# Performance work log

Measured on AMD Instinct MI355X. Metric: run time of the kernel, lower is better.

The kernel has to match this reference:

```python
import jax, jax.numpy as jnp
import numpy as np

D_MODEL = 1024
NHEAD = 16
HEAD_DIM = D_MODEL // NHEAD
D_FF = 4096
B, S = 2, 2048
LN_EPS = 1e-5


def _linear_params(key, d_out, d_in):
    kw, kb = jax.random.split(key)
    lim = 1.0 / np.sqrt(d_in)
    W = jax.random.uniform(kw, (d_out, d_in), jnp.float32, -lim, lim)
    b = jax.random.uniform(kb, (d_out,), jnp.float32, -lim, lim)
    return W, b


def setup_inputs() -> dict:
    key = jax.random.key(0)
    ks = jax.random.split(key, 8)
    src = jax.random.normal(ks[0], (B, S, D_MODEL), jnp.float32)
    mask = jax.random.randint(ks[1], (B, S), 0, 2).astype(bool)
    Wq, bq = _linear_params(ks[2], D_MODEL, D_MODEL)
    Wk, bk = _linear_params(ks[3], D_MODEL, D_MODEL)
    Wv, bv = _linear_params(ks[4], D_MODEL, D_MODEL)
    Wo, bo = _linear_params(ks[5], D_MODEL, D_MODEL)
    W1, b1 = _linear_params(ks[6], D_FF, D_MODEL)
    W2, b2 = _linear_params(ks[7], D_MODEL, D_FF)
    ln1_g = jnp.ones((D_MODEL,), jnp.float32)
    ln1_b = jnp.zeros((D_MODEL,), jnp.float32)
    ln2_g = jnp.ones((D_MODEL,), jnp.float32)
    ln2_b = jnp.zeros((D_MODEL,), jnp.float32)
    return dict(src=src, mask=mask, Wq=Wq, bq=bq, Wk=Wk, bk=bk, Wv=Wv, bv=bv,
                Wo=Wo, bo=bo, W1=W1, b1=b1, W2=W2, b2=b2,
                ln1_g=ln1_g, ln1_b=ln1_b, ln2_g=ln2_g, ln2_b=ln2_b)


def _layernorm(x, g, b):
    mu = jnp.mean(x, axis=-1, keepdims=True)
    var = jnp.mean(jnp.square(x - mu), axis=-1, keepdims=True)
    return (x - mu) * jax.lax.rsqrt(var + LN_EPS) * g + b


def reference(src, mask, Wq, bq, Wk, bk, Wv, bv, Wo, bo, W1, b1, W2, b2,
              ln1_g, ln1_b, ln2_g, ln2_b):
    batch, seq, _ = src.shape
    src_norm = _layernorm(src, ln1_g, ln1_b)
    # projections (torch Linear: x @ W.T + b), split heads -> [B,H,S,Dh]
    def proj(W, b):
        y = jnp.einsum('bsi,oi->bso', src_norm, W) + b
        return y.reshape(batch, seq, NHEAD, HEAD_DIM).transpose(0, 2, 1, 3)
    q, k, v = proj(Wq, bq), proj(Wk, bk), proj(Wv, bv)
    scores = jnp.einsum('bhqd,bhkd->bhqk', q, k) / np.sqrt(HEAD_DIM)
    scores = jnp.where(mask[:, None, None, :], -10000.0, scores)
    attn_probs = jax.nn.softmax(scores, axis=-1)
    attn_out = jnp.einsum('bhqk,bhkd->bhqd', attn_probs, v)
    attn_out = attn_out.transpose(0, 2, 1, 3).reshape(batch, seq, D_MODEL)
    attn_out = jnp.einsum('bsi,oi->bso', attn_out, Wo) + bo
    src = src + attn_out
    src_norm2 = _layernorm(src, ln2_g, ln2_b)
    h = jax.nn.relu(jnp.einsum('bsi,oi->bso', src_norm2, W1) + b1)
    ff = jnp.einsum('bsi,oi->bso', h, W2) + b2
    src = src + ff
    return (src, attn_probs)
```

## Files before the change

kernel.cpp:

```cpp
#include <hip/hip_runtime.h>
#include <math.h>

typedef __bf16 bf16;
typedef __bf16 bf16x4 __attribute__((ext_vector_type(4)));
typedef __bf16 bf16x8 __attribute__((ext_vector_type(8)));
typedef float f32x4 __attribute__((ext_vector_type(4)));

__device__ __forceinline__ f32x4 mfma16(bf16x8 a, bf16x8 b, f32x4 c) {
  return __builtin_amdgcn_mfma_f32_16x16x32_bf16(a, b, c, 0, 0, 0);
}

__device__ __forceinline__ void gload_lds16(const void* g, void* l) {
  __builtin_amdgcn_global_load_lds((__attribute__((address_space(1))) void*)(g),
                                   (__attribute__((address_space(3))) void*)(l),
                                   16, 0, 0);
}

__global__ __launch_bounds__(256)
void cvt_all(const float* __restrict__ Wq, const float* __restrict__ Wk,
             const float* __restrict__ Wv, const float* __restrict__ Wo,
             const float* __restrict__ W1, const float* __restrict__ W2,
             const float* __restrict__ bq, const float* __restrict__ bk,
             const float* __restrict__ bv, bf16* __restrict__ wqkv,
             bf16* __restrict__ wob, bf16* __restrict__ w1b,
             bf16* __restrict__ w2b, float* __restrict__ bqkv) {
  const int i = blockIdx.x * 256 + threadIdx.x;
  if (i < 3145728) {
    float4 v;
    bf16* dst;
    size_t di;
    if (i < 262144) { v = ((const float4*)Wq)[i]; dst = wqkv; di = i; }
    else if (i < 524288) { v = ((const float4*)Wk)[i - 262144]; dst = wqkv; di = i; }
    else if (i < 786432) { v = ((const float4*)Wv)[i - 524288]; dst = wqkv; di = i; }
    else if (i < 1048576) { v = ((const float4*)Wo)[i - 786432]; dst = wob; di = i - 786432; }
    else if (i < 2097152) { v = ((const float4*)W1)[i - 1048576]; dst = w1b; di = i - 1048576; }
    else { v = ((const float4*)W2)[i - 2097152]; dst = w2b; di = i - 2097152; }
    bf16x4 o;
    o[0] = (bf16)v.x; o[1] = (bf16)v.y; o[2] = (bf16)v.z; o[3] = (bf16)v.w;
    reinterpret_cast<bf16x4*>(dst)[di] = o;
  } else {
    const int j = i - 3145728;
    const float* s = (j < 256) ? bq : ((j < 512) ? bk : bv);
    reinterpret_cast<float4*>(bqkv)[j] = reinterpret_cast<const float4*>(s)[j & 255];
  }
}

__global__ __launch_bounds__(256)
void ln_bf16(const float* __restrict__ x, const float* __restrict__ g,
             const float* __restrict__ bta, bf16* __restrict__ y) {
  const int row = blockIdx.x, t = threadIdx.x;
  const float4 v = reinterpret_cast<const float4*>(x)[(size_t)row * 256 + t];
  float s1 = v.x + v.y + v.z + v.w;
  float s2 = v.x * v.x + v.y * v.y + v.z * v.z + v.w * v.w;
#pragma unroll
  for (int m = 1; m < 64; m <<= 1) {
    s1 += __shfl_xor(s1, m);
    s2 += __shfl_xor(s2, m);
  }
  __shared__ float red[8];
  if ((t & 63) == 0) { red[(t >> 6) * 2] = s1; red[(t >> 6) * 2 + 1] = s2; }
  __syncthreads();
  s1 = red[0] + red[2] + red[4] + red[6];
  s2 = red[1] + red[3] + red[5] + red[7];
  const float mu = s1 * (1.f / 1024.f);
  const float rs = rsqrtf(s2 * (1.f / 1024.f) - mu * mu + 1e-5f);
  const float4 gv = reinterpret_cast<const float4*>(g)[t];
  const float4 bv = reinterpret_cast<const float4*>(bta)[t];
  bf16x4 o;
  o[0] = (bf16)((v.x - mu) * rs * gv.x + bv.x);
  o[1] = (bf16)((v.y - mu) * rs * gv.y + bv.y);
  o[2] = (bf16)((v.z - mu) * rs * gv.z + bv.z);
  o[3] = (bf16)((v.w - mu) * rs * gv.w + bv.w);
  reinterpret_cast<bf16x4*>(y)[(size_t)row * 256 + t] = o;
}

__global__ __launch_bounds__(256)
void tr_v(const bf16* __restrict__ QKV, bf16* __restrict__ VT) {
  __shared__ bf16 T[64 * 80];
  const int t = threadIdx.x;
  const int sb = blockIdx.x * 64, h = blockIdx.y, b = blockIdx.z;
  const int srow = t >> 2, c16 = t & 3;
  const bf16* src = QKV + (size_t)(b * 2048 + sb + srow) * 3072 + 2048 + h * 64 + c16 * 16;
  bf16x8 a0 = *reinterpret_cast<const bf16x8*>(src);
  bf16x8 a1 = *reinterpret_cast<const bf16x8*>(src + 8);
  *reinterpret_cast<bf16x8*>(&T[srow * 80 + c16 * 16]) = a0;
  *reinterpret_cast<bf16x8*>(&T[srow * 80 + c16 * 16 + 8]) = a1;
  __syncthreads();
  const int drow = t >> 2, sq = t & 3;
  bf16x8 o0, o1;
#pragma unroll
  for (int j = 0; j < 8; ++j) o0[j] = T[(sq * 16 + j) * 80 + drow];
#pragma unroll
  for (int j = 0; j < 8; ++j) o1[j] = T[(sq * 16 + 8 + j) * 80 + drow];
  bf16* dst = VT + ((size_t)(b * 16 + h) * 64 + drow) * 2048 + sb + sq * 16;
  *reinterpret_cast<bf16x8*>(dst) = o0;
  *reinterpret_cast<bf16x8*>(dst + 8) = o1;
}

template <int TM, bool OUT_BF16, bool RELU, bool RES, bool QSC>
__global__ __launch_bounds__(256)
void gemm_bt(const bf16* __restrict__ A, const bf16* __restrict__ Bw,
             const float* __restrict__ bias, const float* __restrict__ res,
             void* __restrict__ Cout, int M, int N, int K) {
  constexpr int MR = TM / 32;
  constexpr int ACH = TM / 64;
  __shared__ bf16 As[3][TM * 32];
  __shared__ bf16 Bs[3][128 * 32];
  const int t = threadIdx.x, wave = t >> 6, lane = t & 63;
  const int l15 = lane & 15, lhi = lane >> 4;
  const int nwg = gridDim.x * gridDim.y;
  const int orig = blockIdx.y * gridDim.x + blockIdx.x;
  const int wgid = (orig & 7) * (nwg >> 3) + (orig >> 3);
  const int bx = wgid % gridDim.x, by = wgid / gridDim.x;
  const int m0 = by * TM, n0 = bx * 128;
  const int wm = (wave >> 1) * (TM / 2), wn = (wave & 1) * 64;
  const f32x4 z4 = {0.f, 0.f, 0.f, 0.f};
  f32x4 acc[MR][4];
#pragma unroll
  for (int m = 0; m < MR; ++m)
#pragma unroll
    for (int n = 0; n < 4; ++n) acc[m][n] = z4;

  int soff[2], srow[2], scol[2];
#pragma unroll
  for (int i = 0; i < 2; ++i) {
    soff[i] = (i * 4 + wave) * 1024 + lane * 16;
    srow[i] = soff[i] >> 6;
    scol[i] = (soff[i] & 63) >> 1;
  }

#define GEMM_STAGE(k0, bb)                                                    \
  do {                                                                        \
    _Pragma("unroll")                                                         \
    for (int i = 0; i < ACH; ++i)                                             \
      gload_lds16(A + (size_t)(m0 + srow[i]) * K + (k0) + scol[i],            \
                  (char*)As[bb] + soff[i]);                                   \
    _Pragma("unroll")                                                         \
    for (int i = 0; i < 2; ++i)                                               \
      gload_lds16(Bw + (size_t)(n0 + srow[i]) * K + (k0) + scol[i],           \
                  (char*)Bs[bb] + soff[i]);                                   \
  } while (0)

  const int nt = K >> 5;
  GEMM_STAGE(0, 0);
  GEMM_STAGE(32, 1);
  if constexpr (TM == 128)
    asm volatile("s_waitcnt vmcnt(4)" ::: "memory");
  else
    asm volatile("s_waitcnt vmcnt(3)" ::: "memory");
  __builtin_amdgcn_s_barrier();

  for (int kt = 0; kt < nt; ++kt) {
    if (kt + 2 < nt) GEMM_STAGE((kt + 2) * 32, (kt + 2) % 3);
    const bf16* Ac = As[kt % 3];
    const bf16* Bc = Bs[kt % 3];
    bf16x8 af[MR], bfr[4];
#pragma unroll
    for (int m = 0; m < MR; ++m)
      af[m] = *reinterpret_cast<const bf16x8*>(&Ac[(wm + m * 16 + l15) * 32 + lhi * 8]);
#pragma unroll
    for (int n = 0; n < 4; ++n)
      bfr[n] = *reinterpret_cast<const bf16x8*>(&Bc[(wn + n * 16 + l15) * 32 + lhi * 8]);
    __builtin_amdgcn_s_setprio(1);
#pragma unroll
    for (int m = 0; m < MR; ++m)
#pragma unroll
      for (int n = 0; n < 4; ++n) acc[m][n] = mfma16(af[m], bfr[n], acc[m][n]);
    __builtin_amdgcn_s_setprio(0);
    if (kt + 1 < nt) {
      if (kt + 2 < nt) {
        if constexpr (TM == 128)
          asm volatile("s_waitcnt vmcnt(4)" ::: "memory");
        else
          asm volatile("s_waitcnt vmcnt(3)" ::: "memory");
      } else {
        asm volatile("s_waitcnt vmcnt(0)" ::: "memory");
      }
      __builtin_amdgcn_s_barrier();
    }
  }
#undef GEMM_STAGE

  const float sc = (QSC && n0 < 1024) ? 0.18033688011112042f : 1.0f;
#pragma unroll
  for (int m = 0; m < MR; ++m) {
    const int row_base = m0 + wm + m * 16 + lhi * 4;
#pragma unroll
    for (int n = 0; n < 4; ++n) {
      const int col = n0 + wn + n * 16 + l15;
      const float bv = bias[col];
#pragma unroll
      for (int r = 0; r < 4; ++r) {
        const int row = row_base + r;
        float v = (acc[m][n][r] + bv) * sc;
        if (RELU) v = v > 0.f ? v : 0.f;
        if (RES) v += res[(size_t)row * N + col];
        if (OUT_BF16)
          ((bf16*)Cout)[(size_t)row * N + col] = (bf16)v;
        else
          ((float*)Cout)[(size_t)row * N + col] = v;
      }
    }
  }
}

__global__ __launch_bounds__(512)
void attn_fused2(const bf16* __restrict__ Qp, const bf16* __restrict__ Kp,
                 const bf16* __restrict__ VTp, const int* __restrict__ mask,
                 float* __restrict__ probs, bf16* __restrict__ Ob) {
  constexpr int S = 2048, LD = 3072, KB = 128, NT = S / KB;
  __shared__ bf16 Kt[KB * 64];
  __shared__ bf16 Vt[64 * KB];
  __shared__ bf16 P[128 * KB];
  __shared__ float msk2[2][KB];
  const int t = threadIdx.x, wave = t >> 6, lane = t & 63;
  const int l15 = lane & 15, lhi = lane >> 4;
  const int flat = blockIdx.x + 16 * (blockIdx.y + 16 * blockIdx.z);
  const int wg = (flat & 7) * 64 + (flat >> 3);
  const int q0 = (wg & 15) * 128, h = (wg >> 4) & 15, b = wg >> 8;
  const int* mrow = mask + b * S;
  const f32x4 z4 = {0.f, 0.f, 0.f, 0.f};

  const bf16* kgp[2];
  const bf16* vgp[2];
  int soff[2];
#pragma unroll
  for (int i = 0; i < 2; ++i) {
    const int off = (i * 8 + wave) * 1024 + lane * 16;
    soff[i] = off;
    const int krow = off >> 7, kbin = off & 127;
    kgp[i] = Kp + (size_t)(b * S + krow) * LD + h * 64 + ((kbin ^ ((krow & 7) << 4)) >> 1);
    const int d = off >> 8, vbin = off & 255;
    vgp[i] = VTp + (size_t)((b * 16 + h) * 64 + d) * S + ((vbin ^ ((d & 7) << 4)) >> 1);
  }

  bf16x8 qf[2];
#pragma unroll
  for (int ks = 0; ks < 2; ++ks)
    qf[ks] = *reinterpret_cast<const bf16x8*>(
        Qp + (size_t)(b * S + q0 + wave * 16 + l15) * LD + h * 64 + ks * 32 + lhi * 8);

  bf16x8 kreg[2];
  float mnext;
#pragma unroll
  for (int i = 0; i < 2; ++i) kreg[i] = *reinterpret_cast<const bf16x8*>(kgp[i]);
  mnext = (t < KB) ? (mrow[t] ? 0.f : 1.f) : 0.f;
#pragma unroll
  for (int i = 0; i < 2; ++i)
    *reinterpret_cast<bf16x8*>((char*)Kt + soff[i]) = kreg[i];
  if (t < KB) msk2[0][t] = mnext;
  __syncthreads();

  float lpart = 0.f;
  for (int kt = 0; kt < NT; ++kt) {
    const int kv0 = kt * KB;
    if (kt + 1 < NT) {
#pragma unroll
      for (int i = 0; i < 2; ++i)
        kreg[i] = *reinterpret_cast<const bf16x8*>(kgp[i] + (size_t)(kv0 + KB) * LD);
      mnext = (t < KB) ? (mrow[kv0 + KB + t] ? 0.f : 1.f) : 0.f;
    }
    const char* kb = (kt & 1) ? (const char*)Vt : (const char*)Kt;
    const float* mc = msk2[kt & 1];
    f32x4 sa[8];
#pragma unroll
    for (int n = 0; n < 8; ++n) sa[n] = z4;
    __builtin_amdgcn_s_setprio(1);
#pragma unroll
    for (int ks = 0; ks < 2; ++ks)
#pragma unroll
      for (int n = 0; n < 8; ++n) {
        const int krow = n * 16 + l15;
        bf16x8 kf = *reinterpret_cast<const bf16x8*>(
            kb + krow * 128 + ((ks * 64 + lhi * 16) ^ ((krow & 7) << 4)));
        sa[n] = mfma16(kf, qf[ks], sa[n]);
      }
    __builtin_amdgcn_s_setprio(0);
#pragma unroll
    for (int n = 0; n < 8; ++n)
#pragma unroll
      for (int r = 0; r < 4; ++r)
        lpart += __builtin_exp2f(sa[n][r]) * mc[n * 16 + lhi * 4 + r];
    if (kt + 1 < NT) {
      char* kbn = ((kt + 1) & 1) ? (char*)Vt : (char*)Kt;
#pragma unroll
      for (int i = 0; i < 2; ++i)
        *reinterpret_cast<bf16x8*>(kbn + soff[i]) = kreg[i];
      if (t < KB) msk2[(kt + 1) & 1][t] = mnext;
    }
    __syncthreads();
  }
  lpart += __shfl_xor(lpart, 16);
  lpart += __shfl_xor(lpart, 32);
  const float il = 1.f / lpart;

  f32x4 oa[4];
#pragma unroll
  for (int n = 0; n < 4; ++n) oa[n] = z4;
  float* pbase = probs + ((size_t)(b * 16 + h) * S + q0 + wave * 16 + l15) * S;
  const int prw = wave * 16 + l15;

  bf16x8 vreg[2];
#pragma unroll
  for (int i = 0; i < 2; ++i) {
    kreg[i] = *reinterpret_cast<const bf16x8*>(kgp[i]);
    vreg[i] = *reinterpret_cast<const bf16x8*>(vgp[i]);
  }
  mnext = (t < KB) ? (mrow[t] ? 0.f : 1.f) : 0.f;
#pragma unroll
  for (int i = 0; i < 2; ++i) {
    *reinterpret_cast<bf16x8*>((char*)Kt + soff[i]) = kreg[i];
    *reinterpret_cast<bf16x8*>((char*)Vt + soff[i]) = vreg[i];
  }
  if (t < KB) msk2[0][t] = mnext;
  __syncthreads();

  for (int kt = 0; kt < NT; ++kt) {
    const int kv0 = kt * KB;
    if (kt + 1 < NT) {
#pragma unroll
      for (int i = 0; i < 2; ++i) {
        kreg[i] = *reinterpret_cast<const bf16x8*>(kgp[i] + (size_t)(kv0 + KB) * LD);
        vreg[i] = *reinterpret_cast<const bf16x8*>(vgp[i] + kv0 + KB);
      }
      mnext = (t < KB) ? (mrow[kv0 + KB + t] ? 0.f : 1.f) : 0.f;
    }

    f32x4 sa[8];
#pragma unroll
    for (int n = 0; n < 8; ++n) sa[n] = z4;
    __builtin_amdgcn_s_setprio(1);
#pragma unroll
    for (int ks = 0; ks < 2; ++ks)
#pragma unroll
      for (int n = 0; n < 8; ++n) {
        const int krow = n * 16 + l15;
        bf16x8 kf = *reinterpret_cast<const bf16x8*>(
            (char*)Kt + krow * 128 + ((ks * 64 + lhi * 16) ^ ((krow & 7) << 4)));
        sa[n] = mfma16(kf, qf[ks], sa[n]);
      }
    __builtin_amdgcn_s_setprio(0);

#pragma unroll
    for (int n = 0; n < 8; ++n) {
      f32x4 praw, pn;
#pragma unroll
      for (int r = 0; r < 4; ++r) {
        praw[r] = __builtin_exp2f(sa[n][r]) * msk2[0][n * 16 + lhi * 4 + r];
        pn[r] = praw[r] * il;
      }
      __builtin_nontemporal_store(pn, reinterpret_cast<f32x4*>(pbase + kv0 + n * 16 + lhi * 4));
      bf16x4 pb;
      pb[0] = (bf16)praw[0]; pb[1] = (bf16)praw[1];
      pb[2] = (bf16)praw[2]; pb[3] = (bf16)praw[3];
      *reinterpret_cast<bf16x4*>(
          (char*)P + prw * 256 + ((n * 32 + lhi * 8) ^ ((prw & 7) << 4))) = pb;
    }
    __builtin_amdgcn_s_setprio(1);
#pragma unroll
    for (int ks = 0; ks < 4; ++ks) {
      bf16x8 pf = *reinterpret_cast<const bf16x8*>(
          (char*)P + prw * 256 + ((ks * 64 + lhi * 16) ^ ((prw & 7) << 4)));
#pragma unroll
      for (int nn = 0; nn < 4; ++nn) {
        const int vr = nn * 16 + l15;
        bf16x8 vf = *reinterpret_cast<const bf16x8*>(
            (char*)Vt + vr * 256 + ((ks * 64 + lhi * 16) ^ ((vr & 7) << 4)));
        oa[nn] = mfma16(pf, vf, oa[nn]);
      }
    }
    __builtin_amdgcn_s_setprio(0);
    __syncthreads();
    if (kt + 1 < NT) {
#pragma unroll
      for (int i = 0; i < 2; ++i) {
        *reinterpret_cast<bf16x8*>((char*)Kt + soff[i]) = kreg[i];
        *reinterpret_cast<bf16x8*>((char*)Vt + soff[i]) = vreg[i];
      }
      if (t < KB) msk2[0][t] = mnext;
    }
    __syncthreads();
  }

  float il4[4];
#pragma unroll
  for (int r = 0; r < 4; ++r) il4[r] = __shfl(il, lhi * 4 + r);
#pragma unroll
  for (int nn = 0; nn < 4; ++nn)
#pragma unroll
    for (int r = 0; r < 4; ++r)
      Ob[(size_t)(b * S + q0 + wave * 16 + lhi * 4 + r) * 1024 + h * 64 + nn * 16 + l15] =
          (bf16)(oa[nn][r] * il4[r]);
}

extern "C" void kernel_launch(void* const* d_in, const int* in_sizes, int n_in,
                              void* d_out, int out_size, void* d_ws, size_t ws_size,
                              hipStream_t stream) {
  const float* src = (const float*)d_in[0];
  const int* mask = (const int*)d_in[1];
  const float* Wq = (const float*)d_in[2];
  const float* bq = (const float*)d_in[3];
  const float* Wk = (const float*)d_in[4];
  const float* bk = (const float*)d_in[5];
  const float* Wv = (const float*)d_in[6];
  const float* bv = (const float*)d_in[7];
  const float* Wo = (const float*)d_in[8];
  const float* bo = (const float*)d_in[9];
  const float* W1 = (const float*)d_in[10];
  const float* b1 = (const float*)d_in[11];
  const float* W2 = (const float*)d_in[12];
  const float* b2 = (const float*)d_in[13];
  const float* ln1g = (const float*)d_in[14];
  const float* ln1b = (const float*)d_in[15];
  const float* ln2g = (const float*)d_in[16];
  const float* ln2b = (const float*)d_in[17];

  float* out0 = (float*)d_out;
  float* probs = (float*)d_out + (size_t)4194304;

  char* w = (char*)d_ws;
  const size_t MB = 1u << 20;
  bf16* wqkv = (bf16*)(w);
  bf16* wob = (bf16*)(w + 6 * MB);
  bf16* w1b = (bf16*)(w + 8 * MB);
  bf16* w2b = (bf16*)(w + 16 * MB);
  bf16* xn = (bf16*)(w + 24 * MB);
  bf16* QKV = (bf16*)(w + 32 * MB);
  bf16* Ob = (bf16*)(w + 56 * MB);
  bf16* hb = (bf16*)(w + 32 * MB);
  bf16* VT = (bf16*)(w + 64 * MB);
  float* s2 = (float*)(w + 64 * MB);
  float* bqkv = (float*)(w + 80 * MB);

  cvt_all<<<12291, 256, 0, stream>>>(Wq, Wk, Wv, Wo, W1, W2, bq, bk, bv,
                                     wqkv, wob, w1b, w2b, bqkv);

  ln_bf16<<<4096, 256, 0, stream>>>(src, ln1g, ln1b, xn);
  gemm_bt<128, true, false, false, true><<<dim3(24, 32), 256, 0, stream>>>(
      xn, wqkv, bqkv, nullptr, QKV, 4096, 3072, 1024);
  tr_v<<<dim3(32, 16, 2), 256, 0, stream>>>(QKV, VT);
  attn_fused2<<<dim3(16, 16, 2), 512, 0, stream>>>(
      QKV, QKV + 1024, VT, mask, probs, Ob);
  gemm_bt<64, false, false, true, false><<<dim3(8, 64), 256, 0, stream>>>(
      Ob, wob, bo, src, s2, 4096, 1024, 1024);
  ln_bf16<<<4096, 256, 0, stream>>>(s2, ln2g, ln2b, xn);
  gemm_bt<128, true, true, false, false><<<dim3(32, 32), 256, 0, stream>>>(
      xn, w1b, b1, nullptr, hb, 4096, 4096, 1024);
  gemm_bt<64, false, false, true, false><<<dim3(8, 64), 256, 0, stream>>>(
      hb, w2b, b2, s2, out0, 4096, 1024, 4096);

  (void)in_sizes; (void)n_in; (void)out_size; (void)ws_size;
}
```

Measured before the change: 424.4 us.

## Add 128x256-tile 512-thread GEMM for QKV and FFN1 projections

Adds a new bf16 GEMM kernel with a 128x256 output tile, 8 waves of 64x64 each, and triple-buffered LDS via direct global-to-LDS loads. It replaces the 128x128 GEMM for the QKV projection and the first FFN layer. The goal is more data reuse per LDS load and fewer workgroups. The trade-off is fewer blocks (384 and 512 on 256 CUs), which can cause tail imbalance, plus more register pressure.

```diff
diff --git a/kernel.cpp b/kernel.cpp
--- a/kernel.cpp
+++ b/kernel.cpp
@@ -97,6 +97,105 @@
   *reinterpret_cast<bf16x8*>(dst + 8) = o1;
 }
 
+template <bool RELU, bool QSC>
+__global__ __launch_bounds__(512)
+void gemm_bt3(const bf16* __restrict__ A, const bf16* __restrict__ Bw,
+              const float* __restrict__ bias, bf16* __restrict__ Cout,
+              int M, int N, int K) {
+  __shared__ bf16 As[3][128 * 32];
+  __shared__ bf16 Bs[3][256 * 32];
+  const int t = threadIdx.x, wave = t >> 6, lane = t & 63;
+  const int l15 = lane & 15, lhi = lane >> 4;
+  const int nwg = gridDim.x * gridDim.y;
+  const int orig = blockIdx.y * gridDim.x + blockIdx.x;
+  const int wgid = (orig & 7) * (nwg >> 3) + (orig >> 3);
+  const int bx = wgid % gridDim.x, by = wgid / gridDim.x;
+  const int m0 = by * 128, n0 = bx * 256;
+  const int wm = (wave >> 2) * 64, wn = (wave & 3) * 64;
+  const f32x4 z4 = {0.f, 0.f, 0.f, 0.f};
+  f32x4 acc[4][4];
+#pragma unroll
+  for (int m = 0; m < 4; ++m)
+#pragma unroll
+    for (int n = 0; n < 4; ++n) acc[m][n] = z4;
+
+  const int da = t * 16;
+  const int ra = da >> 6, ca = (da & 63) ^ ((ra & 3) << 4);
+  const bf16* agp = A + (size_t)(m0 + ra) * K + (ca >> 1);
+  int db_[2], rb_[2];
+  const bf16* bgp[2];
+#pragma unroll
+  for (int j = 0; j < 2; ++j) {
+    db_[j] = j * 8192 + t * 16;
+    rb_[j] = db_[j] >> 6;
+    const int cb = (db_[j] & 63) ^ ((rb_[j] & 3) << 4);
+    bgp[j] = Bw + (size_t)(n0 + rb_[j]) * K + (cb >> 1);
+  }
+
+#define G3_STAGE(k0, bb)                                                      \
+  do {                                                                        \
+    gload_lds16(agp + (k0), (char*)As[bb] + da);                              \
+    gload_lds16(bgp[0] + (k0), (char*)Bs[bb] + db_[0]);                       \
+    gload_lds16(bgp[1] + (k0), (char*)Bs[bb] + db_[1]);                       \
+  } while (0)
+
+  const int nt = K >> 5;
+  G3_STAGE(0, 0);
+  G3_STAGE(32, 1);
+  asm volatile("s_waitcnt vmcnt(3)" ::: "memory");
+  __builtin_amdgcn_s_barrier();
+
+  for (int kt = 0; kt < nt; ++kt) {
+    if (kt + 2 < nt) G3_STAGE((kt + 2) * 32, (kt + 2) % 3);
+    const char* Ac = (const char*)As[kt % 3];
+    const char* Bc = (const char*)Bs[kt % 3];
+    bf16x8 af[4], bfr[4];
+#pragma unroll
+    for (int m = 0; m < 4; ++m) {
+      const int row = wm + m * 16 + l15;
+      af[m] = *reinterpret_cast<const bf16x8*>(
+          Ac + row * 64 + ((lhi * 16) ^ ((row & 3) << 4)));
+    }
+#pragma unroll
+    for (int n = 0; n < 4; ++n) {
+      const int row = wn + n * 16 + l15;
+      bfr[n] = *reinterpret_cast<const bf16x8*>(
+          Bc + row * 64 + ((lhi * 16) ^ ((row & 3) << 4)));
+    }
+    __builtin_amdgcn_s_setprio(1);
+#pragma unroll
+    for (int m = 0; m < 4; ++m)
+#pragma unroll
+      for (int n = 0; n < 4; ++n) acc[m][n] = mfma16(af[m], bfr[n], acc[m][n]);
+    __builtin_amdgcn_s_setprio(0);
+    if (kt + 1 < nt) {
+      if (kt + 2 < nt)
+        asm volatile("s_waitcnt vmcnt(3)" ::: "memory");
+      else
+        asm volatile("s_waitcnt vmcnt(0)" ::: "memory");
+      __builtin_amdgcn_s_barrier();
+    }
+  }
+#undef G3_STAGE
+
+  const float sc = (QSC && n0 < 1024) ? 0.18033688011112042f : 1.0f;
+#pragma unroll
+  for (int m = 0; m < 4; ++m) {
+    const int row_base = m0 + wm + m * 16 + lhi * 4;
+#pragma unroll
+    for (int n = 0; n < 4; ++n) {
+      const int col = n0 + wn + n * 16 + l15;
+      const float bv = bias[col];
+#pragma unroll
+      for (int r = 0; r < 4; ++r) {
+        float v = (acc[m][n][r] + bv) * sc;
+        if (RELU) v = v > 0.f ? v : 0.f;
+        Cout[(size_t)(row_base + r) * N + col] = (bf16)v;
+      }
+    }
+  }
+}
+
 template <int TM, bool OUT_BF16, bool RELU, bool RES, bool QSC>
 __global__ __launch_bounds__(256)
 void gemm_bt(const bf16* __restrict__ A, const bf16* __restrict__ Bw,
@@ -436,16 +535,16 @@
                                      wqkv, wob, w1b, w2b, bqkv);
 
   ln_bf16<<<4096, 256, 0, stream>>>(src, ln1g, ln1b, xn);
-  gemm_bt<128, true, false, false, true><<<dim3(24, 32), 256, 0, stream>>>(
-      xn, wqkv, bqkv, nullptr, QKV, 4096, 3072, 1024);
+  gemm_bt3<false, true><<<dim3(12, 32), 512, 0, stream>>>(
+      xn, wqkv, bqkv, QKV, 4096, 3072, 1024);
   tr_v<<<dim3(32, 16, 2), 256, 0, stream>>>(QKV, VT);
   attn_fused2<<<dim3(16, 16, 2), 512, 0, stream>>>(
       QKV, QKV + 1024, VT, mask, probs, Ob);
   gemm_bt<64, false, false, true, false><<<dim3(8, 64), 256, 0, stream>>>(
       Ob, wob, bo, src, s2, 4096, 1024, 1024);
   ln_bf16<<<4096, 256, 0, stream>>>(s2, ln2g, ln2b, xn);
-  gemm_bt<128, true, true, false, false><<<dim3(32, 32), 256, 0, stream>>>(
-      xn, w1b, b1, nullptr, hb, 4096, 4096, 1024);
+  gemm_bt3<true, false><<<dim3(16, 32), 512, 0, stream>>>(
+      xn, w1b, b1, hb, 4096, 4096, 1024);
   gemm_bt<64, false, false, true, false><<<dim3(8, 64), 256, 0, stream>>>(
       hb, w2b, b2, s2, out0, 4096, 1024, 4096);
 
```

After: 408.6 us. -3.7%, faster.
